# Kernel optimization log

Measured on AMD Instinct MI355X. Metric: run time of the kernel, lower is better.

## Reference

```python
import jax, jax.numpy as jnp
import numpy as np

N = 50000          # nodes
E = 800000         # edges (before self-loops)
F_IN = 128         # num_features
HEADS = 4
OUT = 128 // HEADS # per-head channels = num_hidden // heads
NEG_SLOPE = 0.2    # PyG GATConv default


def setup_inputs() -> dict:
    key = jax.random.key(0)
    ks = jax.random.split(key, 10)
    x = jax.random.normal(ks[0], (N, F_IN), jnp.float32)
    edge_index = jax.random.randint(ks[1], (2, E), 0, N, dtype=jnp.int64)
    sW = 1.0 / np.sqrt(F_IN)
    sA = 1.0 / np.sqrt(OUT)
    return {
        "x": x,
        "edge_index": edge_index,
        "W1": jax.random.normal(ks[2], (F_IN, HEADS * OUT), jnp.float32) * sW,
        "a_src1": jax.random.normal(ks[3], (HEADS, OUT), jnp.float32) * sA,
        "a_dst1": jax.random.normal(ks[4], (HEADS, OUT), jnp.float32) * sA,
        "b1": jnp.zeros((HEADS * OUT,), jnp.float32),
        "W2": jax.random.normal(ks[5], (HEADS * OUT, HEADS * OUT), jnp.float32) * sW,
        "a_src2": jax.random.normal(ks[6], (HEADS, OUT), jnp.float32) * sA,
        "a_dst2": jax.random.normal(ks[7], (HEADS, OUT), jnp.float32) * sA,
        "b2": jnp.zeros((HEADS * OUT,), jnp.float32),
    }


def gat_conv(x, src, dst, W, a_src, a_dst, b):
    """One GATConv layer (PyG semantics, concat heads, self-loops already in src/dst)."""
    n = x.shape[0]
    h = (x @ W).reshape(n, HEADS, OUT)                 # [N, H, C]
    # per-node attention halves, gathered per edge -> [Etot, H]
    alpha = (h * a_src).sum(-1)[src] + (h * a_dst).sum(-1)[dst]
    alpha = jax.nn.leaky_relu(alpha, NEG_SLOPE)
    # softmax over incoming edges of each destination node (stable)
    amax = jax.ops.segment_max(alpha, dst, num_segments=n)
    ex = jnp.exp(alpha - amax[dst])
    denom = jax.ops.segment_sum(ex, dst, num_segments=n)
    attn = ex / (denom[dst] + 1e-16)                    # [Etot, H]
    # weighted message scatter-add
    out = jax.ops.segment_sum(h[src] * attn[..., None], dst, num_segments=n)
    return out.reshape(n, HEADS * OUT) + b


def reference(x, edge_index, W1, a_src1, a_dst1, b1, W2, a_src2, a_dst2, b2):
    loops = jnp.arange(N, dtype=edge_index.dtype)       # PyG add_self_loops=True
    src = jnp.concatenate([edge_index[0], loops])
    dst = jnp.concatenate([edge_index[1], loops])
    h = jax.nn.relu(gat_conv(x, src, dst, W1, a_src1, a_dst1, b1))
    # dropout = identity in eval mode
    h = jax.nn.relu(gat_conv(h, src, dst, W2, a_src2, a_dst2, b2))
    return h
```

## Files before the change

### kernel.cpp

```cpp
#include <hip/hip_runtime.h>
#include <hip/hip_fp16.h>
#include <cstdint>
#include <cstddef>

#define NN 50000
#define EE 800000
#define ETOT (EE + NN)
#define FD 128
#define NH 4
#define NEG_SLOPE 0.2f

#define BSHIFT 10
#define BSIZE 1024
#define NBKT ((NN + BSIZE - 1) / BSIZE)
#define CAPG 20000
#define CHUNK 2048
#define P1_BLOCKS ((ETOT + CHUNK - 1) / CHUNK)

typedef _Float16 half8 __attribute__((ext_vector_type(8)));
typedef float f32x4 __attribute__((ext_vector_type(4)));


__global__ void zero_kernel(int* __restrict__ gcnt) {
    int t = threadIdx.x;
    if (t < NBKT) gcnt[t] = 0;
}


__global__ __launch_bounds__(256) void bin_kernel(const int* __restrict__ ei,
                                                  int* __restrict__ gcnt,
                                                  uint32_t* __restrict__ gbkt,
                                                  const float* __restrict__ W1,
                                                  const float* __restrict__ W2,
                                                  uint4* __restrict__ Wf1,
                                                  uint4* __restrict__ Wf2) {
    if (blockIdx.x >= P1_BLOCKS) {
        const float* W = (blockIdx.x - P1_BLOCKS) ? W2 : W1;
        uint4* Wf = (blockIdx.x - P1_BLOCKS) ? Wf2 : Wf1;
        for (int s = threadIdx.x; s < 2048; s += 256) {
            int fi = s >> 6;
            int lane = s & 63;
            int ct = fi >> 2, ks = fi & 3;
            int col = ct * 16 + (lane & 15);
            int kb = ks * 32 + (lane >> 4) * 8;
            half8 h;
            #pragma unroll
            for (int j = 0; j < 8; ++j) h[j] = (_Float16)W[(kb + j) * FD + col];
            Wf[s] = *(uint4*)&h;
        }
        return;
    }
    __shared__ int lcnt[NBKT];
    __shared__ int gb[NBKT];
    const int t = threadIdx.x;
    if (t < NBKT) lcnt[t] = 0;
    __syncthreads();
    const int base = blockIdx.x * CHUNK;
    uint32_t pk[8]; int bk[8]; int sl[8];
    #pragma unroll
    for (int j = 0; j < 8; ++j) {
        int e = base + j * 256 + t;
        bk[j] = -1;
        if (e < ETOT) {
            int src, dst;
            if (e < EE) { src = ei[e]; dst = ei[EE + e]; }
            else        { src = e - EE; dst = src; }
            int b = dst >> BSHIFT;
            bk[j] = b;
            pk[j] = (uint32_t)src | ((uint32_t)(dst & (BSIZE - 1)) << 16);
            sl[j] = atomicAdd(&lcnt[b], 1);
        }
    }
    __syncthreads();
    if (t < NBKT) gb[t] = atomicAdd(&gcnt[t], lcnt[t]);
    __syncthreads();
    #pragma unroll
    for (int j = 0; j < 8; ++j)
        if (bk[j] >= 0)
            gbkt[(size_t)bk[j] * CAPG + gb[bk[j]] + sl[j]] = pk[j];
}


__global__ __launch_bounds__(1024) void sort_kernel(const int* __restrict__ gcnt,
                                                    const uint32_t* __restrict__ gbkt,
                                                    int* __restrict__ row_ptr,
                                                    int* __restrict__ csr) {
    __shared__ int cnt[BSIZE];
    __shared__ int pfx[BSIZE];
    __shared__ int wsum[16];
    __shared__ int sCbase;
    const int b = blockIdx.x;
    const int t = threadIdx.x;
    const int count = gcnt[b];
    const int dstBase = b << BSHIFT;
    const int ndst = (NN - dstBase < BSIZE) ? (NN - dstBase) : BSIZE;
    const uint32_t* mybkt = gbkt + (size_t)b * CAPG;
    cnt[t] = 0;
    if (t < 64) {
        int v = (t < NBKT) ? gcnt[t] : 0;
        int inc = v;
        #pragma unroll
        for (int off = 1; off < 64; off <<= 1) {
            int u = __shfl_up(inc, off);
            if (t >= off) inc += u;
        }
        if (t == b) sCbase = inc - v;
    }
    __syncthreads();
    const int cbase = sCbase;
    for (int i = t; i < count; i += 1024)
        atomicAdd(&cnt[mybkt[i] >> 16], 1);
    __syncthreads();
    int v = cnt[t];
    int inc = v;
    const int lane = t & 63, wid = t >> 6;
    #pragma unroll
    for (int off = 1; off < 64; off <<= 1) {
        int u = __shfl_up(inc, off);
        if (lane >= off) inc += u;
    }
    if (lane == 63) wsum[wid] = inc;
    __syncthreads();
    if (t < 16) {
        int w = wsum[t]; int wi = w;
        #pragma unroll
        for (int off = 1; off < 16; off <<= 1) {
            int u = __shfl_up(wi, off);
            if (t >= off) wi += u;
        }
        wsum[t] = wi - w;
    }
    __syncthreads();
    int excl = wsum[wid] + inc - v;
    pfx[t] = excl;
    if (t < ndst) row_ptr[dstBase + t] = cbase + excl;
    if (b == NBKT - 1 && t == 0) row_ptr[NN] = ETOT;
    cnt[t] = 0;
    __syncthreads();
    for (int i = t; i < count; i += 1024) {
        uint32_t pkv = mybkt[i];
        int dl = pkv >> 16;
        int r = atomicAdd(&cnt[dl], 1);
        csr[cbase + pfx[dl] + r] = (int)(pkv & 0xFFFFu);
    }
}


__global__ __launch_bounds__(256) void gemm_kernel(const float* __restrict__ X,
                                                   const uint4* __restrict__ Wf,
                                                   __half* __restrict__ Hh) {
    const int tid = threadIdx.x;
    const int wv = tid >> 6, lane = tid & 63;
    const int l15 = lane & 15, lg = lane >> 4;
    const int rowA = blockIdx.x * 64 + wv * 16 + l15;
    const int rA = (rowA < NN) ? rowA : NN - 1;
    half8 a[4];
    #pragma unroll
    for (int ks = 0; ks < 4; ++ks) {
        int kb = ks * 32 + lg * 8;
        float4 x0 = *(const float4*)&X[(size_t)rA * FD + kb];
        float4 x1 = *(const float4*)&X[(size_t)rA * FD + kb + 4];
        a[ks][0] = (_Float16)x0.x; a[ks][1] = (_Float16)x0.y;
        a[ks][2] = (_Float16)x0.z; a[ks][3] = (_Float16)x0.w;
        a[ks][4] = (_Float16)x1.x; a[ks][5] = (_Float16)x1.y;
        a[ks][6] = (_Float16)x1.z; a[ks][7] = (_Float16)x1.w;
    }
    const int rowC = blockIdx.x * 64 + wv * 16 + lg * 4;
    #pragma unroll
    for (int ct = 0; ct < 8; ++ct) {
        uint4 braw[4];
        #pragma unroll
        for (int ks = 0; ks < 4; ++ks) braw[ks] = Wf[(ct * 4 + ks) * 64 + lane];
        f32x4 acc = {0.f, 0.f, 0.f, 0.f};
        #pragma unroll
        for (int ks = 0; ks < 4; ++ks) {
            half8 b = *(half8*)&braw[ks];
            acc = __builtin_amdgcn_mfma_f32_16x16x32_f16(a[ks], b, acc, 0, 0, 0);
        }
        #pragma unroll
        for (int r = 0; r < 4; ++r) {
            int gr = rowC + r;
            if (gr < NN) Hh[(size_t)gr * FD + ct * 16 + l15] = __float2half(acc[r]);
        }
    }
}


__global__ __launch_bounds__(256) void adot_kernel(const __half* __restrict__ H,
                                                   const float* __restrict__ a_src,
                                                   const float* __restrict__ a_dst,
                                                   float* __restrict__ AS,
                                                   float* __restrict__ AD) {
    int gt = blockIdx.x * 256 + threadIdx.x;
    int n = gt >> 4;
    int l = gt & 15;
    if (n >= NN) return;
    union { uint4 u; __half2 q[4]; } hv;
    hv.u = *(const uint4*)&H[(size_t)n * FD + l * 8];
    float ps = 0.f, pd = 0.f;
    #pragma unroll
    for (int j = 0; j < 4; ++j) {
        float2 f = __half22float2(hv.q[j]);
        ps += f.x * a_src[l * 8 + 2 * j] + f.y * a_src[l * 8 + 2 * j + 1];
        pd += f.x * a_dst[l * 8 + 2 * j] + f.y * a_dst[l * 8 + 2 * j + 1];
    }
    ps += __shfl_xor(ps, 1); ps += __shfl_xor(ps, 2);
    pd += __shfl_xor(pd, 1); pd += __shfl_xor(pd, 2);
    if ((l & 3) == 0) {
        AS[n * NH + (l >> 2)] = ps;
        AD[n * NH + (l >> 2)] = pd;
    }
}


__global__ __launch_bounds__(256) void agg_kernel(const __half* __restrict__ H,
                                                  const float* __restrict__ AS,
                                                  const float* __restrict__ AD,
                                                  const int* __restrict__ row_ptr,
                                                  const int* __restrict__ csr_src,
                                                  const float* __restrict__ bias,
                                                  float* __restrict__ Out) {
    __shared__ float sP[8][32][4];
    __shared__ int   sS[8][32];
    const int wave = threadIdx.x >> 6;
    const int lane = threadIdx.x & 63;
    const int sub  = lane >> 5;
    const int sl   = lane & 31;
    const int ws   = wave * 2 + sub;
    const int n = blockIdx.x * 8 + ws;
    const int start = row_ptr[n], end = row_ptr[n + 1];
    const int h0 = sl >> 3;
    const float4 adv = *(const float4*)&AD[n * NH];
    float spm = 0.f;
    float acc0 = 0.f, acc1 = 0.f, acc2 = 0.f, acc3 = 0.f;

    for (int base = start; base < end; base += 32) {
        int cn = end - base; if (cn > 32) cn = 32;
        int my_src = 0;
        float al[NH] = {0.f, 0.f, 0.f, 0.f};
        if (sl < cn) {
            my_src = csr_src[base + sl];
            float4 asv = *(const float4*)&AS[my_src * NH];
            al[0] = asv.x + adv.x; al[1] = asv.y + adv.y;
            al[2] = asv.z + adv.z; al[3] = asv.w + adv.w;
        }
        sS[ws][sl] = my_src;
        float4 pv;
        {
            float a0 = (al[0] > 0.f) ? al[0] : NEG_SLOPE * al[0];
            float a1 = (al[1] > 0.f) ? al[1] : NEG_SLOPE * al[1];
            float a2 = (al[2] > 0.f) ? al[2] : NEG_SLOPE * al[2];
            float a3 = (al[3] > 0.f) ? al[3] : NEG_SLOPE * al[3];
            pv.x = __expf(a0); pv.y = __expf(a1);
            pv.z = __expf(a2); pv.w = __expf(a3);
        }
        *(float4*)&sP[ws][sl][0] = pv;
        #pragma unroll 4
        for (int e = 0; e < cn; ++e) {
            float pm = sP[ws][e][h0];
            int se = sS[ws][e];
            union { uint2 u; __half2 q[2]; } hv;
            hv.u = *(const uint2*)&H[(size_t)se * FD + sl * 4];
            float2 f0 = __half22float2(hv.q[0]);
            float2 f1 = __half22float2(hv.q[1]);
            acc0 += pm * f0.x; acc1 += pm * f0.y;
            acc2 += pm * f1.x; acc3 += pm * f1.y;
            spm  += pm;
        }
    }
    float inv = 1.f / (spm + 1e-16f);
    const float4 bv = *(const float4*)&bias[sl * 4];
    float4 ov;
    ov.x = fmaxf(acc0 * inv + bv.x, 0.f);
    ov.y = fmaxf(acc1 * inv + bv.y, 0.f);
    ov.z = fmaxf(acc2 * inv + bv.z, 0.f);
    ov.w = fmaxf(acc3 * inv + bv.w, 0.f);
    *(float4*)&Out[(size_t)n * FD + sl * 4] = ov;
}


extern "C" void kernel_launch(void* const* d_in, const int* in_sizes, int n_in,
                              void* d_out, int out_size, void* d_ws, size_t ws_size,
                              hipStream_t stream) {
    const float* x     = (const float*)d_in[0];
    const int*   ei    = (const int*)d_in[1];
    const float* W1    = (const float*)d_in[2];
    const float* asrc1 = (const float*)d_in[3];
    const float* adst1 = (const float*)d_in[4];
    const float* b1    = (const float*)d_in[5];
    const float* W2    = (const float*)d_in[6];
    const float* asrc2 = (const float*)d_in[7];
    const float* adst2 = (const float*)d_in[8];
    const float* b2    = (const float*)d_in[9];
    float* out = (float*)d_out;

    char* p = (char*)d_ws;
    auto alloc = [&](size_t bytes) {
        char* q = p;
        p += (bytes + 255) & ~(size_t)255;
        return q;
    };
    int*      row_ptr = (int*)alloc((NN + 1) * sizeof(int));
    int*      gcnt    = (int*)alloc(NBKT * sizeof(int));
    uint32_t* gbkt    = (uint32_t*)alloc((size_t)NBKT * CAPG * sizeof(uint32_t));
    int*      csr     = (int*)alloc((size_t)ETOT * sizeof(int));
    float*    AS      = (float*)alloc((size_t)NN * NH * sizeof(float));
    float*    AD      = (float*)alloc((size_t)NN * NH * sizeof(float));
    __half*   Hh      = (__half*)alloc((size_t)NN * FD * sizeof(__half));
    uint4*    Wf1     = (uint4*)alloc(2048 * sizeof(uint4));
    uint4*    Wf2     = (uint4*)alloc(2048 * sizeof(uint4));
    (void)ws_size; (void)in_sizes; (void)n_in; (void)out_size;

    zero_kernel<<<1, 64, 0, stream>>>(gcnt);
    bin_kernel<<<P1_BLOCKS + 2, 256, 0, stream>>>(ei, gcnt, gbkt, W1, W2, Wf1, Wf2);
    sort_kernel<<<NBKT, 1024, 0, stream>>>(gcnt, gbkt, row_ptr, csr);

    gemm_kernel<<<(NN + 63) / 64, 256, 0, stream>>>(x, Wf1, Hh);
    adot_kernel<<<(NN * 16 + 255) / 256, 256, 0, stream>>>(Hh, asrc1, adst1, AS, AD);
    agg_kernel<<<NN / 8, 256, 0, stream>>>(Hh, AS, AD, row_ptr, csr, b1, out);

    gemm_kernel<<<(NN + 63) / 64, 256, 0, stream>>>(out, Wf2, Hh);
    adot_kernel<<<(NN * 16 + 255) / 256, 256, 0, stream>>>(Hh, asrc2, adst2, AS, AD);
    agg_kernel<<<NN / 8, 256, 0, stream>>>(Hh, AS, AD, row_ptr, csr, b2, out);
}
```

Before: 142.0 us.

## Merge independent graph-build and layer-1 kernels to cut launch count

The zero and weight-pack steps move into one init kernel. The layer-1 GEMM is folded into the edge-binning launch as extra blocks, and the layer-1 attention dot is folded into the CSR sort launch as extra 1024-thread blocks. Launches drop from nine to seven, and independent work (graph binning and the dense GEMM) can run concurrently on the GPU. In exchange, the sort launch now carries adot blocks with a 1024-thread launch bound and the sort kernel's shared-memory footprint, which may lower occupancy for that part.

```diff
diff --git a/kernel.cpp b/kernel.cpp
--- a/kernel.cpp
+++ b/kernel.cpp
@@ -16,38 +16,111 @@
 #define CAPG 20000
 #define CHUNK 2048
 #define P1_BLOCKS ((ETOT + CHUNK - 1) / CHUNK)
+#define GEMM_BLOCKS ((NN + 63) / 64)
+#define ADOT_BLOCKS ((NN * 16 + 1023) / 1024)
 
 typedef _Float16 half8 __attribute__((ext_vector_type(8)));
 typedef float f32x4 __attribute__((ext_vector_type(4)));
 
 
-__global__ void zero_kernel(int* __restrict__ gcnt) {
-    int t = threadIdx.x;
-    if (t < NBKT) gcnt[t] = 0;
-}
-
-
-__global__ __launch_bounds__(256) void bin_kernel(const int* __restrict__ ei,
-                                                  int* __restrict__ gcnt,
-                                                  uint32_t* __restrict__ gbkt,
-                                                  const float* __restrict__ W1,
-                                                  const float* __restrict__ W2,
-                                                  uint4* __restrict__ Wf1,
-                                                  uint4* __restrict__ Wf2) {
+__device__ __forceinline__ void gemm_body(const float* __restrict__ X,
+                                          const uint4* __restrict__ Wf,
+                                          __half* __restrict__ Hh,
+                                          int bidx, int tid) {
+    const int wv = tid >> 6, lane = tid & 63;
+    const int l15 = lane & 15, lg = lane >> 4;
+    const int rowA = bidx * 64 + wv * 16 + l15;
+    const int rA = (rowA < NN) ? rowA : NN - 1;
+    half8 a[4];
+    #pragma unroll
+    for (int ks = 0; ks < 4; ++ks) {
+        int kb = ks * 32 + lg * 8;
+        float4 x0 = *(const float4*)&X[(size_t)rA * FD + kb];
+        float4 x1 = *(const float4*)&X[(size_t)rA * FD + kb + 4];
+        a[ks][0] = (_Float16)x0.x; a[ks][1] = (_Float16)x0.y;
+        a[ks][2] = (_Float16)x0.z; a[ks][3] = (_Float16)x0.w;
+        a[ks][4] = (_Float16)x1.x; a[ks][5] = (_Float16)x1.y;
+        a[ks][6] = (_Float16)x1.z; a[ks][7] = (_Float16)x1.w;
+    }
+    const int rowC = bidx * 64 + wv * 16 + lg * 4;
+    #pragma unroll
+    for (int ct = 0; ct < 8; ++ct) {
+        uint4 braw[4];
+        #pragma unroll
+        for (int ks = 0; ks < 4; ++ks) braw[ks] = Wf[(ct * 4 + ks) * 64 + lane];
+        f32x4 acc = {0.f, 0.f, 0.f, 0.f};
+        #pragma unroll
+        for (int ks = 0; ks < 4; ++ks) {
+            half8 b = *(half8*)&braw[ks];
+            acc = __builtin_amdgcn_mfma_f32_16x16x32_f16(a[ks], b, acc, 0, 0, 0);
+        }
+        #pragma unroll
+        for (int r = 0; r < 4; ++r) {
+            int gr = rowC + r;
+            if (gr < NN) Hh[(size_t)gr * FD + ct * 16 + l15] = __float2half(acc[r]);
+        }
+    }
+}
+
+__device__ __forceinline__ void adot_body(const __half* __restrict__ H,
+                                          const float* __restrict__ a_src,
+                                          const float* __restrict__ a_dst,
+                                          float* __restrict__ AS,
+                                          float* __restrict__ AD, int gt) {
+    int n = gt >> 4;
+    int l = gt & 15;
+    if (n >= NN) return;
+    union { uint4 u; __half2 q[4]; } hv;
+    hv.u = *(const uint4*)&H[(size_t)n * FD + l * 8];
+    float ps = 0.f, pd = 0.f;
+    #pragma unroll
+    for (int j = 0; j < 4; ++j) {
+        float2 f = __half22float2(hv.q[j]);
+        ps += f.x * a_src[l * 8 + 2 * j] + f.y * a_src[l * 8 + 2 * j + 1];
+        pd += f.x * a_dst[l * 8 + 2 * j] + f.y * a_dst[l * 8 + 2 * j + 1];
+    }
+    ps += __shfl_xor(ps, 1); ps += __shfl_xor(ps, 2);
+    pd += __shfl_xor(pd, 1); pd += __shfl_xor(pd, 2);
+    if ((l & 3) == 0) {
+        AS[n * NH + (l >> 2)] = ps;
+        AD[n * NH + (l >> 2)] = pd;
+    }
+}
+
+
+__global__ __launch_bounds__(256) void init_kernel(int* __restrict__ gcnt,
+                                                   const float* __restrict__ W1,
+                                                   const float* __restrict__ W2,
+                                                   uint4* __restrict__ Wf1,
+                                                   uint4* __restrict__ Wf2) {
+    if (blockIdx.x == 0) {
+        if (threadIdx.x < NBKT) gcnt[threadIdx.x] = 0;
+        return;
+    }
+    const float* W = (blockIdx.x == 2) ? W2 : W1;
+    uint4* Wf = (blockIdx.x == 2) ? Wf2 : Wf1;
+    for (int s = threadIdx.x; s < 2048; s += 256) {
+        int fi = s >> 6;
+        int lane = s & 63;
+        int ct = fi >> 2, ks = fi & 3;
+        int col = ct * 16 + (lane & 15);
+        int kb = ks * 32 + (lane >> 4) * 8;
+        half8 h;
+        #pragma unroll
+        for (int j = 0; j < 8; ++j) h[j] = (_Float16)W[(kb + j) * FD + col];
+        Wf[s] = *(uint4*)&h;
+    }
+}
+
+
+__global__ __launch_bounds__(256) void binGemm_kernel(const int* __restrict__ ei,
+                                                      int* __restrict__ gcnt,
+                                                      uint32_t* __restrict__ gbkt,
+                                                      const float* __restrict__ X,
+                                                      const uint4* __restrict__ Wf1,
+                                                      __half* __restrict__ Hh) {
     if (blockIdx.x >= P1_BLOCKS) {
-        const float* W = (blockIdx.x - P1_BLOCKS) ? W2 : W1;
-        uint4* Wf = (blockIdx.x - P1_BLOCKS) ? Wf2 : Wf1;
-        for (int s = threadIdx.x; s < 2048; s += 256) {
-            int fi = s >> 6;
-            int lane = s & 63;
-            int ct = fi >> 2, ks = fi & 3;
-            int col = ct * 16 + (lane & 15);
-            int kb = ks * 32 + (lane >> 4) * 8;
-            half8 h;
-            #pragma unroll
-            for (int j = 0; j < 8; ++j) h[j] = (_Float16)W[(kb + j) * FD + col];
-            Wf[s] = *(uint4*)&h;
-        }
+        gemm_body(X, Wf1, Hh, blockIdx.x - P1_BLOCKS, threadIdx.x);
         return;
     }
     __shared__ int lcnt[NBKT];
@@ -81,10 +154,20 @@
 }
 
 
-__global__ __launch_bounds__(1024) void sort_kernel(const int* __restrict__ gcnt,
-                                                    const uint32_t* __restrict__ gbkt,
-                                                    int* __restrict__ row_ptr,
-                                                    int* __restrict__ csr) {
+__global__ __launch_bounds__(1024) void sortAdot_kernel(const int* __restrict__ gcnt,
+                                                        const uint32_t* __restrict__ gbkt,
+                                                        int* __restrict__ row_ptr,
+                                                        int* __restrict__ csr,
+                                                        const __half* __restrict__ Hh,
+                                                        const float* __restrict__ a_src,
+                                                        const float* __restrict__ a_dst,
+                                                        float* __restrict__ AS,
+                                                        float* __restrict__ AD) {
+    if (blockIdx.x >= NBKT) {
+        adot_body(Hh, a_src, a_dst, AS, AD,
+                  (blockIdx.x - NBKT) * 1024 + threadIdx.x);
+        return;
+    }
     __shared__ int cnt[BSIZE];
     __shared__ int pfx[BSIZE];
     __shared__ int wsum[16];
@@ -149,67 +232,15 @@
 __global__ __launch_bounds__(256) void gemm_kernel(const float* __restrict__ X,
                                                    const uint4* __restrict__ Wf,
                                                    __half* __restrict__ Hh) {
-    const int tid = threadIdx.x;
-    const int wv = tid >> 6, lane = tid & 63;
-    const int l15 = lane & 15, lg = lane >> 4;
-    const int rowA = blockIdx.x * 64 + wv * 16 + l15;
-    const int rA = (rowA < NN) ? rowA : NN - 1;
-    half8 a[4];
-    #pragma unroll
-    for (int ks = 0; ks < 4; ++ks) {
-        int kb = ks * 32 + lg * 8;
-        float4 x0 = *(const float4*)&X[(size_t)rA * FD + kb];
-        float4 x1 = *(const float4*)&X[(size_t)rA * FD + kb + 4];
-        a[ks][0] = (_Float16)x0.x; a[ks][1] = (_Float16)x0.y;
-        a[ks][2] = (_Float16)x0.z; a[ks][3] = (_Float16)x0.w;
-        a[ks][4] = (_Float16)x1.x; a[ks][5] = (_Float16)x1.y;
-        a[ks][6] = (_Float16)x1.z; a[ks][7] = (_Float16)x1.w;
-    }
-    const int rowC = blockIdx.x * 64 + wv * 16 + lg * 4;
-    #pragma unroll
-    for (int ct = 0; ct < 8; ++ct) {
-        uint4 braw[4];
-        #pragma unroll
-        for (int ks = 0; ks < 4; ++ks) braw[ks] = Wf[(ct * 4 + ks) * 64 + lane];
-        f32x4 acc = {0.f, 0.f, 0.f, 0.f};
-        #pragma unroll
-        for (int ks = 0; ks < 4; ++ks) {
-            half8 b = *(half8*)&braw[ks];
-            acc = __builtin_amdgcn_mfma_f32_16x16x32_f16(a[ks], b, acc, 0, 0, 0);
-        }
-        #pragma unroll
-        for (int r = 0; r < 4; ++r) {
-            int gr = rowC + r;
-            if (gr < NN) Hh[(size_t)gr * FD + ct * 16 + l15] = __float2half(acc[r]);
-        }
-    }
-}
-
+    gemm_body(X, Wf, Hh, blockIdx.x, threadIdx.x);
+}
 
 __global__ __launch_bounds__(256) void adot_kernel(const __half* __restrict__ H,
                                                    const float* __restrict__ a_src,
                                                    const float* __restrict__ a_dst,
                                                    float* __restrict__ AS,
                                                    float* __restrict__ AD) {
-    int gt = blockIdx.x * 256 + threadIdx.x;
-    int n = gt >> 4;
-    int l = gt & 15;
-    if (n >= NN) return;
-    union { uint4 u; __half2 q[4]; } hv;
-    hv.u = *(const uint4*)&H[(size_t)n * FD + l * 8];
-    float ps = 0.f, pd = 0.f;
-    #pragma unroll
-    for (int j = 0; j < 4; ++j) {
-        float2 f = __half22float2(hv.q[j]);
-        ps += f.x * a_src[l * 8 + 2 * j] + f.y * a_src[l * 8 + 2 * j + 1];
-        pd += f.x * a_dst[l * 8 + 2 * j] + f.y * a_dst[l * 8 + 2 * j + 1];
-    }
-    ps += __shfl_xor(ps, 1); ps += __shfl_xor(ps, 2);
-    pd += __shfl_xor(pd, 1); pd += __shfl_xor(pd, 2);
-    if ((l & 3) == 0) {
-        AS[n * NH + (l >> 2)] = ps;
-        AD[n * NH + (l >> 2)] = pd;
-    }
+    adot_body(H, a_src, a_dst, AS, AD, blockIdx.x * 256 + threadIdx.x);
 }
 
 
@@ -311,15 +342,12 @@
     uint4*    Wf2     = (uint4*)alloc(2048 * sizeof(uint4));
     (void)ws_size; (void)in_sizes; (void)n_in; (void)out_size;
 
-    zero_kernel<<<1, 64, 0, stream>>>(gcnt);
-    bin_kernel<<<P1_BLOCKS + 2, 256, 0, stream>>>(ei, gcnt, gbkt, W1, W2, Wf1, Wf2);
-    sort_kernel<<<NBKT, 1024, 0, stream>>>(gcnt, gbkt, row_ptr, csr);
-
-    gemm_kernel<<<(NN + 63) / 64, 256, 0, stream>>>(x, Wf1, Hh);
-    adot_kernel<<<(NN * 16 + 255) / 256, 256, 0, stream>>>(Hh, asrc1, adst1, AS, AD);
+    init_kernel<<<3, 256, 0, stream>>>(gcnt, W1, W2, Wf1, Wf2);
+    binGemm_kernel<<<P1_BLOCKS + GEMM_BLOCKS, 256, 0, stream>>>(ei, gcnt, gbkt, x, Wf1, Hh);
+    sortAdot_kernel<<<NBKT + ADOT_BLOCKS, 1024, 0, stream>>>(gcnt, gbkt, row_ptr, csr,
+                                                             Hh, asrc1, adst1, AS, AD);
     agg_kernel<<<NN / 8, 256, 0, stream>>>(Hh, AS, AD, row_ptr, csr, b1, out);
-
-    gemm_kernel<<<(NN + 63) / 64, 256, 0, stream>>>(out, Wf2, Hh);
+    gemm_kernel<<<GEMM_BLOCKS, 256, 0, stream>>>(out, Wf2, Hh);
     adot_kernel<<<(NN * 16 + 255) / 256, 256, 0, stream>>>(Hh, asrc2, adst2, AS, AD);
     agg_kernel<<<NN / 8, 256, 0, stream>>>(Hh, AS, AD, row_ptr, csr, b2, out);
 }
```

Result: faster. 133.6 us (-6.0%).
